# Kernel tuning notes

Hardware: AMD Instinct MI355X
Metric: run time of the kernel (lower is better)

The kernel has to match this reference:

```python
import jax, jax.numpy as jnp
import numpy as np

K = 5  # spline kernel size per dim (dim=3 -> 125 kernels)
N1, E1 = 10000, 60000
N2, E2 = 2500, 15000
N3, E3 = 625, 3750
N4, E4 = 160, 960
NC = 4  # num part classes (ShapeNet 'Pistol')


def spline_conv(x, ei, u, W, R, b):
    """SplineConv with degree-1 open B-splines, dim=3, kernel_size=K.
    x: [N, in], ei: [2, E] (src, dst), u: [E, 3] pseudo coords in [0,1],
    W: [K^3, in, out], R: [in, out] root weight, b: [out] bias.
    Mean-normalized neighborhood aggregation (norm=True) + root + bias."""
    src, dst = ei[0], ei[1]
    N, E = x.shape[0], ei.shape[1]
    v = u * (K - 1)
    k0f = jnp.clip(jnp.floor(v), 0.0, K - 2)
    f = v - k0f  # fractional offsets in [0, 1]
    k0 = k0f.astype(jnp.int32)
    # Pre-transform node features by every kernel: z[n, k, o]
    z = jnp.einsum('ni,kio->nko', x, W)
    msg = jnp.zeros((E, W.shape[2]), x.dtype)
    for b0 in (0, 1):
        for b1 in (0, 1):
            for b2 in (0, 1):
                idx = (k0[:, 0] + b0) * K * K + (k0[:, 1] + b1) * K + (k0[:, 2] + b2)
                wgt = ((f[:, 0] if b0 else 1.0 - f[:, 0]) *
                       (f[:, 1] if b1 else 1.0 - f[:, 1]) *
                       (f[:, 2] if b2 else 1.0 - f[:, 2]))
                msg = msg + wgt[:, None] * z[src, idx]
    agg = jax.ops.segment_sum(msg, dst, num_segments=N)
    deg = jax.ops.segment_sum(jnp.ones((E,), x.dtype), dst, num_segments=N)
    return agg / jnp.maximum(deg, 1.0)[:, None] + x @ R + b


def _net(x, u1, u2, u3, u4, w1, r1, b1, w12, r12, b12, w2, r2, b2, w22, r22, b22,
         w3, r3, b3, w32, r32, b32, w4, r4, b4, w42, r42, b42, w5, r5, b5,
         w6, r6, b6, w7, r7, b7, fc1w, fc1b, fc2w, fc2b,
         sk1w, sk1b, sk2w, sk2b, sk3w, sk3b, ei1, ei2, ei3, ei4, c1, c2, c3):
    elu = jax.nn.elu
    h1 = elu(spline_conv(x, ei1, u1, w1, r1, b1))
    h1 = elu(spline_conv(h1, ei1, u1, w12, r12, b12))
    h2 = jnp.concatenate([jax.ops.segment_max(h1, c1, num_segments=N2),
                          jnp.ones((N2, 1), x.dtype)], axis=1)
    h2 = elu(spline_conv(h2, ei2, u2, w2, r2, b2))
    h2 = elu(spline_conv(h2, ei2, u2, w22, r22, b22))
    h3 = jnp.concatenate([jax.ops.segment_max(h2, c2, num_segments=N3),
                          jnp.ones((N3, 1), x.dtype)], axis=1)
    h3 = elu(spline_conv(h3, ei3, u3, w3, r3, b3))
    h3 = elu(spline_conv(h3, ei3, u3, w32, r32, b32))
    h4 = jnp.concatenate([jax.ops.segment_max(h3, c3, num_segments=N4),
                          jnp.ones((N4, 1), x.dtype)], axis=1)
    h4 = elu(spline_conv(h4, ei4, u4, w4, r4, b4))
    h4 = elu(spline_conv(h4, ei4, u4, w42, r42, b42))
    h4 = elu(spline_conv(h4, ei4, u4, w42, r42, b42))  # conv42 applied twice, as in source
    h4 = elu(h4 @ fc1w + fc1b)  # dropout omitted (eval mode)
    g3 = elu(spline_conv(h4[c3] + h3 @ sk3w + sk3b, ei3, u3, w5, r5, b5))
    g2 = elu(spline_conv(g3[c2] + h2 @ sk2w + sk2b, ei2, u2, w6, r6, b6))
    g1 = elu(spline_conv(g2[c1] + h1 @ sk1w + sk1b, ei1, u1, w7, r7, b7))
    return jax.nn.log_softmax(g1 @ fc2w + fc2b, axis=1)


def setup_inputs() -> dict:
    key = jax.random.key(0)
    ks = iter(jax.random.split(key, 96))

    def nrm(shape, s=0.1):
        return jax.random.normal(next(ks), shape, jnp.float32) * s

    def edges(E, N):
        return jax.random.randint(next(ks), (2, E), 0, N, dtype=jnp.int32)

    def clus(Nl, Nn):
        # surjective cluster assignment so every pooled voxel is non-empty
        extra = jax.random.randint(next(ks), (Nl - Nn,), 0, Nn, dtype=jnp.int32)
        return jnp.concatenate([jnp.arange(Nn, dtype=jnp.int32), extra])

    d = {}
    d['x'] = nrm((N1, 1), 1.0)
    d['ei1'], d['u1'] = edges(E1, N1), jax.random.uniform(next(ks), (E1, 3), jnp.float32)
    d['ei2'], d['u2'] = edges(E2, N2), jax.random.uniform(next(ks), (E2, 3), jnp.float32)
    d['ei3'], d['u3'] = edges(E3, N3), jax.random.uniform(next(ks), (E3, 3), jnp.float32)
    d['ei4'], d['u4'] = edges(E4, N4), jax.random.uniform(next(ks), (E4, 3), jnp.float32)
    d['c1'], d['c2'], d['c3'] = clus(N1, N2), clus(N2, N3), clus(N3, N4)
    KK = K ** 3
    for name, cin, cout in [('1', 1, 64), ('12', 64, 64), ('2', 65, 64), ('22', 64, 64),
                            ('3', 65, 64), ('32', 64, 64), ('4', 65, 64), ('42', 64, 64),
                            ('5', 32, 32), ('6', 32, 32), ('7', 32, 32)]:
        d['w' + name] = nrm((KK, cin, cout))
        d['r' + name] = nrm((cin, cout))
        d['b' + name] = jnp.zeros((cout,), jnp.float32)
    d['fc1w'], d['fc1b'] = nrm((64, 32)), jnp.zeros((32,), jnp.float32)
    d['fc2w'], d['fc2b'] = nrm((32, NC)), jnp.zeros((NC,), jnp.float32)
    for s in ('1', '2', '3'):
        d['sk' + s + 'w'] = nrm((64, 32))
        d['sk' + s + 'b'] = jnp.zeros((32,), jnp.float32)
    return d


def reference(x, u1, u2, u3, u4, w1, r1, b1, w12, r12, b12, w2, r2, b2, w22, r22, b22,
              w3, r3, b3, w32, r32, b32, w4, r4, b4, w42, r42, b42, w5, r5, b5,
              w6, r6, b6, w7, r7, b7, fc1w, fc1b, fc2w, fc2b,
              sk1w, sk1b, sk2w, sk2b, sk3w, sk3b, ei1, ei2, ei3, ei4, c1, c2, c3):
    return _net(x, u1, u2, u3, u4, w1, r1, b1, w12, r12, b12, w2, r2, b2, w22, r22, b22,
                w3, r3, b3, w32, r32, b32, w4, r4, b4, w42, r42, b42, w5, r5, b5,
                w6, r6, b6, w7, r7, b7, fc1w, fc1b, fc2w, fc2b,
                sk1w, sk1b, sk2w, sk2b, sk3w, sk3b, ei1, ei2, ei3, ei4, c1, c2, c3)
```

## Files before the change

### kernel.cpp

```cpp
#include <hip/hip_runtime.h>
#include <math.h>


static const int N1 = 10000, E1 = 60000;
static const int N2 = 2500,  E2 = 15000;
static const int N3 = 625,   E3 = 3750;
static const int N4 = 160,   E4 = 960;
static const int NC = 4;
static const int CHUNK = 64;

typedef __attribute__((ext_vector_type(8))) short bfrag;
typedef __attribute__((ext_vector_type(4))) float f32x4;

__device__ __forceinline__ float eluf(float x) { return x > 0.f ? x : expm1f(x); }

__device__ __forceinline__ unsigned short bfc(float f) {
    unsigned u = __float_as_uint(f);
    return (unsigned short)((u + 0x7FFF + ((u >> 16) & 1)) >> 16);
}

struct InitArgs {
    const float* wsrc[10]; unsigned short* wdst[10];
    int cinmat[10], xs_[10], cout[10];
    long welems[10];
    long wtot;
    float* pools[3]; int pM[3];
    float* agg; int aggN4;
    int* preblk; int preN;
    int bB, bC, bD;
};

__global__ __launch_bounds__(256) void init_misc(InitArgs A) {
    const int blk = blockIdx.x, tid = threadIdx.x;
    if (blk < A.bB) {
        const long t = (long)blk * 256 + tid;
        if (t >= A.wtot) return;
        int k = 0;
        while (t >= A.welems[k]) ++k;
        const long base = k ? A.welems[k - 1] : 0;
        const long i2 = t - base;
        const int co = A.cout[k], cm = A.cinmat[k], xs = A.xs_[k];
        const int o = (int)(i2 % co);
        const long rest = i2 / co;
        const int i = (int)(rest % cm);
        const int kk = (int)(rest / cm);
        const float v = A.wsrc[k][((size_t)kk * xs + i) * co + o];
        const int KG = cm >> 3;
        A.wdst[k][(((size_t)(kk * KG + (i >> 3))) * co + o) * 8 + (i & 7)] = bfc(v);
    } else if (blk < A.bC) {
        const int t = (blk - A.bB) * 256 + tid;
        if (t >= A.pM[2]) return;
        const int p = (t < A.pM[0]) ? 0 : (t < A.pM[1] ? 1 : 2);
        const int base = p ? A.pM[p - 1] : 0;
        const int i2 = t - base;
        A.pools[p][i2] = (i2 % 65 == 64) ? 1.0f : -INFINITY;
    } else if (blk < A.bD) {
        const int t = (blk - A.bC) * 256 + tid;
        if (t < A.aggN4) ((float4*)A.agg)[t] = make_float4(0.f, 0.f, 0.f, 0.f);
    } else {
        const int t = (blk - A.bD) * 256 + tid;
        if (t < A.preN) A.preblk[t] = 0;
    }
}

struct Levels {
    const float* u[4]; const int* ei[4]; int E[4];
    int nb0[5];
    int cb0[5];
    int mc[4];
    int* ek0[4]; int* hist[4]; int* cursor[4]; float* deg[4];
    int* bchunk0[4]; int* ck0[4]; int* ccnt[4]; int* perm[4];
};

__global__ __launch_bounds__(256) void prep_all(Levels L) {
    int l = 0;
    while (l < 3 && (int)blockIdx.x >= L.nb0[l + 1]) ++l;
    const int bl = blockIdx.x - L.nb0[l];
    __shared__ int lh[64];
    const int t = threadIdx.x;
    if (t < 64) lh[t] = 0;
    __syncthreads();
    const int e = bl * 256 + t;
    if (e < L.E[l]) {
        int b = 0;
        #pragma unroll
        for (int d = 0; d < 3; ++d) {
            const float v = L.u[l][e * 3 + d] * 4.0f;
            const float kf = fminf(fmaxf(floorf(v), 0.f), 3.f);
            b = (b << 2) | (int)kf;
        }
        L.ek0[l][e] = b;
        atomicAdd(&lh[b], 1);
        atomicAdd(&L.deg[l][L.ei[l][L.E[l] + e]], 1.0f);
    }
    __syncthreads();
    if (t < 64 && lh[t]) atomicAdd(&L.hist[l][t], lh[t]);
}

__global__ void scan_all(Levels L) {
    const int l = blockIdx.x;
    __shared__ int sb[65];
    const int t = threadIdx.x;
    if (t == 0) {
        int cc = 0;
        for (int b = 0; b < 64; ++b) { sb[b] = cc; cc += (L.hist[l][b] + CHUNK - 1) / CHUNK; }
        sb[64] = cc;
    }
    __syncthreads();
    L.bchunk0[l][t] = sb[t];
    if (t == 0) L.bchunk0[l][64] = sb[64];
}

__global__ void fill_chunks_all(Levels L) {
    int l = 0;
    while (l < 3 && (int)blockIdx.x >= L.cb0[l + 1]) ++l;
    const int c = (blockIdx.x - L.cb0[l]) * 256 + threadIdx.x;
    if (c >= L.mc[l]) return;
    const int* bchunk0 = L.bchunk0[l];
    if (c >= bchunk0[64]) { L.ccnt[l][c] = 0; L.ck0[l][c] = 0; return; }
    int lo = 0, hi = 64;
    while (hi - lo > 1) { int m = (lo + hi) >> 1; if (bchunk0[m] <= c) lo = m; else hi = m; }
    const int j = c - bchunk0[lo];
    L.ck0[l][c] = lo;
    L.ccnt[l][c] = min(CHUNK, L.hist[l][lo] - j * CHUNK);
}

__global__ __launch_bounds__(256) void scatter_all(Levels L) {
    int l = 0;
    while (l < 3 && (int)blockIdx.x >= L.nb0[l + 1]) ++l;
    const int bl = blockIdx.x - L.nb0[l];
    __shared__ int lh[64], lbase[64];
    const int t = threadIdx.x;
    if (t < 64) lh[t] = 0;
    __syncthreads();
    const int e = bl * 256 + t;
    int b = -1, r = 0;
    if (e < L.E[l]) { b = L.ek0[l][e]; r = atomicAdd(&lh[b], 1); }
    __syncthreads();
    if (t < 64) lbase[t] = lh[t] ? atomicAdd(&L.cursor[l][t], lh[t]) : 0;
    __syncthreads();
    if (e < L.E[l]) L.perm[l][L.bchunk0[l][b] * CHUNK + lbase[b] + r] = e;
}

template<int CINMAT, int COUT, bool HAS_ONES>
__global__ __launch_bounds__(256) void bucket_gemm(
        const float* __restrict__ x, const int* __restrict__ ei, const float* __restrict__ u,
        const unsigned short* __restrict__ Wt, const float* __restrict__ Wf,
        const int* __restrict__ perm, const int* __restrict__ ck0, const int* __restrict__ ccnt,
        float* __restrict__ agg, int E) {
    constexpr int ALDA = CINMAT + 8;
    constexpr int KG   = CINMAT / 8;
    constexpr int NT   = COUT / 16;
    constexpr int HALVES = CINMAT / 32;
    constexpr int XS   = CINMAT + (HAS_ONES ? 1 : 0);
    constexpr int IT   = CINMAT / 4;

    __shared__ unsigned short A0s[64 * ALDA], A1s[64 * ALDA];
    __shared__ float gS[64 * 4], sS[64 * 2];
    __shared__ int srcS[64], dstS[64];
    __shared__ float WonesS[HAS_ONES ? 8 * COUT : 4];

    const int chunk = blockIdx.x;
    const int cnt = ccnt[chunk];
    if (cnt == 0) return;
    const int b = ck0[chunk];
    const int kbase = ((b >> 4) & 3) * 25 + ((b >> 2) & 3) * 5 + (b & 3);
    const int cstart = chunk * CHUNK;
    const int tid = threadIdx.x;

    if (tid < CHUNK) {
        const int e = tid;
        const int pe = (e < cnt) ? perm[cstart + e] : -1;
        int sv = -1, dv = 0;
        float g0 = 0, g1 = 0, g2 = 0, g3 = 0, s0 = 0, s1 = 0;
        if (pe >= 0) {
            sv = ei[pe]; dv = ei[E + pe];
            float f[3];
            #pragma unroll
            for (int d2 = 0; d2 < 3; ++d2) {
                const float v = u[pe * 3 + d2] * 4.f;
                const float kf = fminf(fmaxf(floorf(v), 0.f), 3.f);
                f[d2] = v - kf;
            }
            g0 = (1.f - f[0]) * (1.f - f[1]); g1 = (1.f - f[0]) * f[1];
            g2 = f[0] * (1.f - f[1]);         g3 = f[0] * f[1];
            s0 = 1.f - f[2]; s1 = f[2];
        }
        srcS[e] = sv; dstS[e] = dv;
        gS[e * 4 + 0] = g0; gS[e * 4 + 1] = g1; gS[e * 4 + 2] = g2; gS[e * 4 + 3] = g3;
        sS[e * 2 + 0] = s0; sS[e * 2 + 1] = s1;
    }
    if (HAS_ONES) {
        for (int t2 = tid; t2 < 8 * COUT; t2 += 256) {
            const int c = t2 / COUT, o = t2 % COUT;
            const int koff = ((c >> 2) & 1) * 25 + ((c >> 1) & 1) * 5 + (c & 1);
            WonesS[t2] = Wf[((size_t)(kbase + koff) * XS + CINMAT) * COUT + o];
        }
    }
    __syncthreads();

    {
        const int e  = tid >> 2;
        const int ib = (tid & 3) * IT;
        const int sv = srcS[e];
        const float sc0 = sS[e * 2], sc1 = sS[e * 2 + 1];
        #pragma unroll
        for (int j = 0; j < IT; j += 2) {
            float x0 = 0.f, x1 = 0.f;
            if (sv >= 0) {
                x0 = x[(size_t)sv * XS + ib + j];
                x1 = x[(size_t)sv * XS + ib + j + 1];
            }
            const unsigned p0 = bfc(x0 * sc0) | ((unsigned)bfc(x1 * sc0) << 16);
            const unsigned p1 = bfc(x0 * sc1) | ((unsigned)bfc(x1 * sc1) << 16);
            *(unsigned*)&A0s[e * ALDA + ib + j] = p0;
            *(unsigned*)&A1s[e * ALDA + ib + j] = p1;
        }
    }
    __syncthreads();

    const int lane = tid & 63;
    const int wid  = tid >> 6;
    const int m0   = wid * 16;
    const int arow = m0 + (lane & 15);
    const int kg   = lane >> 4;
    const int ocol = lane & 15;

    f32x4 acc[4][NT];
    #pragma unroll
    for (int q = 0; q < 4; ++q)
        #pragma unroll
        for (int nt = 0; nt < NT; ++nt) acc[q][nt] = (f32x4){0.f, 0.f, 0.f, 0.f};

    #pragma unroll
    for (int q = 0; q < 4; ++q) {
        #pragma unroll
        for (int b2 = 0; b2 < 2; ++b2) {
            const unsigned short* Ab = b2 ? A1s : A0s;
            const int koff = (q >> 1) * 25 + (q & 1) * 5 + b2;
            #pragma unroll
            for (int hf = 0; hf < HALVES; ++hf) {
                const bfrag a = *(const bfrag*)(Ab + arow * ALDA + hf * 32 + kg * 8);
                const int krow = (kbase + koff) * KG + hf * 4 + kg;
                #pragma unroll
                for (int nt = 0; nt < NT; ++nt) {
                    const bfrag bb = *(const bfrag*)(Wt + ((size_t)krow * COUT + nt * 16 + ocol) * 8);
                    acc[q][nt] = __builtin_amdgcn_mfma_f32_16x16x32_bf16(a, bb, acc[q][nt], 0, 0, 0);
                }
            }
        }
    }

    const int grp = lane >> 4;
    #pragma unroll
    for (int nt = 0; nt < NT; ++nt) {
        const int o = nt * 16 + ocol;
        float wo[8];
        if (HAS_ONES) {
            #pragma unroll
            for (int c = 0; c < 8; ++c) wo[c] = WonesS[c * COUT + o];
        }
        #pragma unroll
        for (int r = 0; r < 4; ++r) {
            const int e = m0 + grp * 4 + r;
            if (e < cnt) {
                const float g0 = gS[e * 4 + 0], g1 = gS[e * 4 + 1];
                const float g2 = gS[e * 4 + 2], g3 = gS[e * 4 + 3];
                float v = g0 * acc[0][nt][r] + g1 * acc[1][nt][r] +
                          g2 * acc[2][nt][r] + g3 * acc[3][nt][r];
                if (HAS_ONES) {
                    const float s0v = sS[e * 2], s1v = sS[e * 2 + 1];
                    v += g0 * (s0v * wo[0] + s1v * wo[1]) + g1 * (s0v * wo[2] + s1v * wo[3]) +
                         g2 * (s0v * wo[4] + s1v * wo[5]) + g3 * (s0v * wo[6] + s1v * wo[7]);
                }
                atomicAdd(&agg[(size_t)dstS[e] * COUT + o], v);
            }
        }
    }
}

template<int CIN, int COUT, int BLK>
__global__ __launch_bounds__(BLK) void bucket_edge(
        const float* __restrict__ x, const int* __restrict__ ei, const float* __restrict__ u,
        const float* __restrict__ W, const int* __restrict__ perm,
        const int* __restrict__ ck0, const int* __restrict__ ccnt,
        float* __restrict__ agg, int E) {
    constexpr int CINP = (CIN + 3) & ~3;
    __shared__ float xs[CHUNK * CINP];
    __shared__ float wgt[CHUNK * 8];
    __shared__ int pel[CHUNK], srcl[CHUNK], dstl[CHUNK];

    const int chunk = blockIdx.x;
    const int cnt = ccnt[chunk];
    if (cnt == 0) return;
    const int b = ck0[chunk];
    const int kbase = ((b >> 4) & 3) * 25 + ((b >> 2) & 3) * 5 + (b & 3);
    const int cstart = chunk * CHUNK;
    const int tid = threadIdx.x;

    for (int e = tid; e < CHUNK; e += BLK) {
        if (e < cnt) {
            const int pe = perm[cstart + e];
            pel[e] = pe; srcl[e] = ei[pe]; dstl[e] = ei[E + pe];
        } else { pel[e] = -1; srcl[e] = -1; dstl[e] = -1; }
    }
    __syncthreads();
    for (int t2 = tid; t2 < CHUNK * 8; t2 += BLK) {
        const int e = t2 >> 3, c = t2 & 7;
        float w = 0.f;
        const int pe = pel[e];
        if (pe >= 0) {
            w = 1.f;
            #pragma unroll
            for (int d = 0; d < 3; ++d) {
                const float v = u[pe * 3 + d] * 4.0f;
                const float kf = fminf(fmaxf(floorf(v), 0.f), 3.f);
                const float fr = v - kf;
                const int bd = (c >> (2 - d)) & 1;
                w *= bd ? fr : 1.f - fr;
            }
        }
        wgt[t2] = w;
    }
    for (int t2 = tid; t2 < CHUNK * CINP; t2 += BLK) {
        const int e = t2 / CINP, i = t2 - e * CINP;
        const int s = srcl[e];
        xs[t2] = (s >= 0 && i < CIN) ? x[(size_t)s * CIN + i] : 0.f;
    }
    __syncthreads();

    const int lane = tid & 63;
    const int wid  = tid >> 6;
    const int o = lane;
    const int ehbase = wid * 8;

    float acc2[8][8];
    #pragma unroll
    for (int c = 0; c < 8; ++c)
        #pragma unroll
        for (int e = 0; e < 8; ++e) acc2[c][e] = 0.f;

    for (int i = 0; i < CIN; ++i) {
        float xr1[8];
        #pragma unroll
        for (int e = 0; e < 8; ++e) xr1[e] = xs[(ehbase + e) * CINP + i];
        #pragma unroll
        for (int c = 0; c < 8; ++c) {
            const int off = ((c >> 2) & 1) * 25 + ((c >> 1) & 1) * 5 + (c & 1);
            const float w0 = W[(size_t)(kbase + off) * (CIN * COUT) + (size_t)i * COUT + o];
            #pragma unroll
            for (int e = 0; e < 8; ++e) acc2[c][e] += xr1[e] * w0;
        }
    }
    #pragma unroll
    for (int e = 0; e < 8; ++e) {
        const int ge = ehbase + e;
        if (ge < cnt) {
            float a = 0.f;
            #pragma unroll
            for (int c = 0; c < 8; ++c) a += wgt[ge * 8 + c] * acc2[c][e];
            atomicAdd(&agg[(size_t)dstl[ge] * COUT + o], a);
        }
    }
}

enum { NODE_PLAIN = 0, NODE_SEGMAX = 1, NODE_LSM = 2 };

template<int CIN, int COUT, int MODE>
__global__ void spline_node_f(const float* __restrict__ x, float* __restrict__ agg,
                              const float* __restrict__ deg, const float* __restrict__ R,
                              const float* __restrict__ b, float* __restrict__ out, int N,
                              const int* __restrict__ cl, float* __restrict__ pool,
                              const float* __restrict__ fcw, const float* __restrict__ fcb,
                              float* __restrict__ lout) {
    constexpr int NPB = 256 / COUT;
    const int lane = threadIdx.x % COUT;
    const int grp  = threadIdx.x / COUT;
    const int n = blockIdx.x * NPB + grp;
    if (n >= N) return;
    const float d = fmaxf(deg[n], 1.f);
    const size_t idx = (size_t)n * COUT + lane;
    float s = agg[idx] / d + b[lane];
    agg[idx] = 0.f;
    const float* xs = x + (size_t)n * CIN;
    #pragma unroll 4
    for (int i = 0; i < CIN; ++i) s += xs[i] * R[i * COUT + lane];
    const float val = eluf(s);
    if (MODE != NODE_LSM) out[idx] = val;
    if (MODE == NODE_SEGMAX) {
        float* addr = pool + (size_t)cl[n] * 65 + lane;
        if (val >= 0.f) atomicMax((int*)addr, __float_as_int(val));
        else            atomicMin((unsigned int*)addr, __float_as_uint(val));
    }
    if (MODE == NODE_LSM) {
        float p[NC];
        #pragma unroll
        for (int o = 0; o < NC; ++o) p[o] = val * fcw[lane * NC + o];
        #pragma unroll
        for (int m = 16; m >= 1; m >>= 1)
            #pragma unroll
            for (int o = 0; o < NC; ++o) p[o] += __shfl_xor(p[o], m, 32);
        #pragma unroll
        for (int o = 0; o < NC; ++o) p[o] += fcb[o];
        const float mx = fmaxf(fmaxf(p[0], p[1]), fmaxf(p[2], p[3]));
        float se = 0.f;
        #pragma unroll
        for (int o = 0; o < NC; ++o) se += expf(p[o] - mx);
        const float lg = logf(se);
        if (lane < NC) lout[(size_t)n * NC + lane] = p[lane] - mx - lg;
    }
}

__global__ void skip_gather(const float* __restrict__ up, const int* __restrict__ cl,
                            const float* __restrict__ h, const float* __restrict__ skw,
                            const float* __restrict__ skb, float* __restrict__ out, int N) {
    const int lane = threadIdx.x & 31;
    const int grp  = threadIdx.x >> 5;
    const int n = blockIdx.x * 8 + grp;
    if (n >= N) return;
    float s = up[(size_t)cl[n] * 32 + lane] + skb[lane];
    const float* hs = h + (size_t)n * 64;
    #pragma unroll 4
    for (int i = 0; i < 64; ++i) s += hs[i] * skw[i * 32 + lane];
    out[(size_t)n * 32 + lane] = s;
}

__global__ void linear_elu_64_32(const float* __restrict__ x, const float* __restrict__ w,
                                 const float* __restrict__ b, float* __restrict__ out, int N) {
    const int lane = threadIdx.x & 31;
    const int grp  = threadIdx.x >> 5;
    const int n = blockIdx.x * 8 + grp;
    if (n >= N) return;
    float s = b[lane];
    const float* xs = x + (size_t)n * 64;
    #pragma unroll 4
    for (int i = 0; i < 64; ++i) s += xs[i] * w[i * 32 + lane];
    out[(size_t)n * 32 + lane] = eluf(s);
}

struct HLevel {
    const int* ei; const float* u; int E; int maxchunks;
    int *ek0, *hist, *cursor, *bchunk0, *ck0, *ccnt, *perm;
    float* deg;
};

extern "C" void kernel_launch(void* const* d_in, const int* in_sizes, int n_in,
                              void* d_out, int out_size, void* d_ws, size_t ws_size,
                              hipStream_t stream) {
    const float* x    = (const float*)d_in[0];
    const int*   ei1  = (const int*)  d_in[1];
    const float* u1   = (const float*)d_in[2];
    const int*   ei2  = (const int*)  d_in[3];
    const float* u2   = (const float*)d_in[4];
    const int*   ei3  = (const int*)  d_in[5];
    const float* u3   = (const float*)d_in[6];
    const int*   ei4  = (const int*)  d_in[7];
    const float* u4   = (const float*)d_in[8];
    const int*   c1   = (const int*)  d_in[9];
    const int*   c2   = (const int*)  d_in[10];
    const int*   c3   = (const int*)  d_in[11];
    const float *w1  = (const float*)d_in[12], *r1  = (const float*)d_in[13], *b1  = (const float*)d_in[14];
    const float *w12 = (const float*)d_in[15], *r12 = (const float*)d_in[16], *b12 = (const float*)d_in[17];
    const float *w2  = (const float*)d_in[18], *r2  = (const float*)d_in[19], *b2  = (const float*)d_in[20];
    const float *w22 = (const float*)d_in[21], *r22 = (const float*)d_in[22], *b22 = (const float*)d_in[23];
    const float *w3  = (const float*)d_in[24], *r3  = (const float*)d_in[25], *b3  = (const float*)d_in[26];
    const float *w32 = (const float*)d_in[27], *r32 = (const float*)d_in[28], *b32 = (const float*)d_in[29];
    const float *w4  = (const float*)d_in[30], *r4  = (const float*)d_in[31], *b4  = (const float*)d_in[32];
    const float *w42 = (const float*)d_in[33], *r42 = (const float*)d_in[34], *b42 = (const float*)d_in[35];
    const float *w5  = (const float*)d_in[36], *r5  = (const float*)d_in[37], *b5  = (const float*)d_in[38];
    const float *w6  = (const float*)d_in[39], *r6  = (const float*)d_in[40], *b6  = (const float*)d_in[41];
    const float *w7  = (const float*)d_in[42], *r7  = (const float*)d_in[43], *b7  = (const float*)d_in[44];
    const float *fc1w = (const float*)d_in[45], *fc1b = (const float*)d_in[46];
    const float *fc2w = (const float*)d_in[47], *fc2b = (const float*)d_in[48];
    const float *sk1w = (const float*)d_in[49], *sk1b = (const float*)d_in[50];
    const float *sk2w = (const float*)d_in[51], *sk2b = (const float*)d_in[52];
    const float *sk3w = (const float*)d_in[53], *sk3b = (const float*)d_in[54];
    float* out = (float*)d_out;

    char* wsb = (char*)d_ws;
    size_t off = 0;
    auto alloc = [&](size_t bytes) {
        void* p = wsb + off; off = (off + bytes + 255) & ~(size_t)255; return p;
    };
    auto allocF = [&](size_t n) { return (float*)alloc(n * 4); };
    auto allocI = [&](size_t n) { return (int*)alloc(n * 4); };
    auto allocH = [&](size_t n) { return (unsigned short*)alloc(n * 2); };

    float* h1a  = allocF((size_t)N1 * 64);
    float* h1   = allocF((size_t)N1 * 64);
    float* h2in = allocF((size_t)N2 * 65);
    float* h2a  = allocF((size_t)N2 * 64);
    float* h2   = allocF((size_t)N2 * 64);
    float* h3in = allocF((size_t)N3 * 65);
    float* h3a  = allocF((size_t)N3 * 64);
    float* h3   = allocF((size_t)N3 * 64);
    float* h4in = allocF((size_t)N4 * 65);
    float* h4a  = allocF((size_t)N4 * 64);
    float* h4b  = allocF((size_t)N4 * 64);
    float* h4c  = allocF((size_t)N4 * 64);
    float* h4   = allocF((size_t)N4 * 32);
    float* g3in = allocF((size_t)N3 * 32);
    float* g3   = allocF((size_t)N3 * 32);
    float* g2in = allocF((size_t)N2 * 32);
    float* g2   = allocF((size_t)N2 * 32);
    float* g1in = allocF((size_t)N1 * 32);
    float* agg  = allocF((size_t)N1 * 64);

    const size_t SZ64 = (size_t)125 * 8 * 64 * 8;
    const size_t SZ32 = (size_t)125 * 4 * 32 * 8;
    unsigned short* t12 = allocH(SZ64);
    unsigned short* t22 = allocH(SZ64);
    unsigned short* t32 = allocH(SZ64);
    unsigned short* t42 = allocH(SZ64);
    unsigned short* t2  = allocH(SZ64);
    unsigned short* t3  = allocH(SZ64);
    unsigned short* t4  = allocH(SZ64);
    unsigned short* t5  = allocH(SZ32);
    unsigned short* t6  = allocH(SZ32);
    unsigned short* t7  = allocH(SZ32);

    HLevel L[4];
    const int*   eis[4] = {ei1, ei2, ei3, ei4};
    const float* us [4] = {u1, u2, u3, u4};
    const int    Es [4] = {E1, E2, E3, E4};
    const int    Ns [4] = {N1, N2, N3, N4};

    int preN = 0;
    for (int l = 0; l < 4; ++l) preN += 128 + Ns[l];
    int* preblk = allocI(preN);
    {
        int c = 0;
        for (int l = 0; l < 4; ++l) {
            L[l].ei = eis[l]; L[l].u = us[l]; L[l].E = Es[l];
            L[l].maxchunks = (Es[l] + CHUNK - 1) / CHUNK + 64;
            L[l].hist = preblk + c; L[l].cursor = preblk + c + 64;
            L[l].deg = (float*)(preblk + c + 128);
            c += 128 + Ns[l];
            L[l].ek0     = allocI(Es[l]);
            L[l].bchunk0 = allocI(65);
            L[l].ck0     = allocI(L[l].maxchunks);
            L[l].ccnt    = allocI(L[l].maxchunks);
            L[l].perm    = allocI((size_t)L[l].maxchunks * CHUNK);
        }
    }

    InitArgs IA;
    {
        const float* srcs[10] = {w12, w22, w32, w42, w2, w3, w4, w5, w6, w7};
        unsigned short* dsts[10] = {t12, t22, t32, t42, t2, t3, t4, t5, t6, t7};
        const int cms[10] = {64,64,64,64,64,64,64,32,32,32};
        const int xss[10] = {64,64,64,64,65,65,65,32,32,32};
        const int cos[10] = {64,64,64,64,64,64,64,32,32,32};
        long cum = 0;
        for (int k = 0; k < 10; ++k) {
            IA.wsrc[k] = srcs[k]; IA.wdst[k] = dsts[k];
            IA.cinmat[k] = cms[k]; IA.xs_[k] = xss[k]; IA.cout[k] = cos[k];
            cum += (long)125 * cms[k] * cos[k];
            IA.welems[k] = cum;
        }
        IA.wtot = cum;
        IA.pools[0] = h2in; IA.pools[1] = h3in; IA.pools[2] = h4in;
        IA.pM[0] = N2 * 65; IA.pM[1] = N2 * 65 + N3 * 65; IA.pM[2] = N2 * 65 + N3 * 65 + N4 * 65;
        IA.agg = agg; IA.aggN4 = N1 * 64 / 4;
        IA.preblk = preblk; IA.preN = preN;
        const int bA = (int)((IA.wtot + 255) / 256);
        const int bB = (IA.pM[2] + 255) / 256;
        const int bC = (IA.aggN4 + 255) / 256;
        const int bD = (preN + 255) / 256;
        IA.bB = bA; IA.bC = bA + bB; IA.bD = bA + bB + bC;
        init_misc<<<bA + bB + bC + bD, 256, 0, stream>>>(IA);
    }

    Levels DL;
    {
        int nb = 0, cb = 0;
        for (int l = 0; l < 4; ++l) {
            DL.u[l] = L[l].u; DL.ei[l] = L[l].ei; DL.E[l] = L[l].E;
            DL.nb0[l] = nb; nb += (L[l].E + 255) / 256;
            DL.cb0[l] = cb; cb += (L[l].maxchunks + 255) / 256;
            DL.mc[l] = L[l].maxchunks;
            DL.ek0[l] = L[l].ek0; DL.hist[l] = L[l].hist; DL.cursor[l] = L[l].cursor;
            DL.deg[l] = L[l].deg; DL.bchunk0[l] = L[l].bchunk0;
            DL.ck0[l] = L[l].ck0; DL.ccnt[l] = L[l].ccnt; DL.perm[l] = L[l].perm;
        }
        DL.nb0[4] = nb; DL.cb0[4] = cb;
        prep_all<<<nb, 256, 0, stream>>>(DL);
        scan_all<<<4, 64, 0, stream>>>(DL);
        fill_chunks_all<<<cb, 256, 0, stream>>>(DL);
        scatter_all<<<nb, 256, 0, stream>>>(DL);
    }

    bucket_edge<1, 64, 512><<<L[0].maxchunks, 512, 0, stream>>>(
        x, L[0].ei, L[0].u, w1, L[0].perm, L[0].ck0, L[0].ccnt, agg, L[0].E);
    spline_node_f<1, 64, NODE_PLAIN><<<(N1 + 3) / 4, 256, 0, stream>>>(
        x, agg, L[0].deg, r1, b1, h1a, N1, nullptr, nullptr, nullptr, nullptr, nullptr);

    bucket_gemm<64, 64, false><<<L[0].maxchunks, 256, 0, stream>>>(
        h1a, L[0].ei, L[0].u, t12, nullptr, L[0].perm, L[0].ck0, L[0].ccnt, agg, L[0].E);
    spline_node_f<64, 64, NODE_SEGMAX><<<(N1 + 3) / 4, 256, 0, stream>>>(
        h1a, agg, L[0].deg, r12, b12, h1, N1, c1, h2in, nullptr, nullptr, nullptr);

    bucket_gemm<64, 64, true><<<L[1].maxchunks, 256, 0, stream>>>(
        h2in, L[1].ei, L[1].u, t2, w2, L[1].perm, L[1].ck0, L[1].ccnt, agg, L[1].E);
    spline_node_f<65, 64, NODE_PLAIN><<<(N2 + 3) / 4, 256, 0, stream>>>(
        h2in, agg, L[1].deg, r2, b2, h2a, N2, nullptr, nullptr, nullptr, nullptr, nullptr);
    bucket_gemm<64, 64, false><<<L[1].maxchunks, 256, 0, stream>>>(
        h2a, L[1].ei, L[1].u, t22, nullptr, L[1].perm, L[1].ck0, L[1].ccnt, agg, L[1].E);
    spline_node_f<64, 64, NODE_SEGMAX><<<(N2 + 3) / 4, 256, 0, stream>>>(
        h2a, agg, L[1].deg, r22, b22, h2, N2, c2, h3in, nullptr, nullptr, nullptr);

    bucket_gemm<64, 64, true><<<L[2].maxchunks, 256, 0, stream>>>(
        h3in, L[2].ei, L[2].u, t3, w3, L[2].perm, L[2].ck0, L[2].ccnt, agg, L[2].E);
    spline_node_f<65, 64, NODE_PLAIN><<<(N3 + 3) / 4, 256, 0, stream>>>(
        h3in, agg, L[2].deg, r3, b3, h3a, N3, nullptr, nullptr, nullptr, nullptr, nullptr);
    bucket_gemm<64, 64, false><<<L[2].maxchunks, 256, 0, stream>>>(
        h3a, L[2].ei, L[2].u, t32, nullptr, L[2].perm, L[2].ck0, L[2].ccnt, agg, L[2].E);
    spline_node_f<64, 64, NODE_SEGMAX><<<(N3 + 3) / 4, 256, 0, stream>>>(
        h3a, agg, L[2].deg, r32, b32, h3, N3, c3, h4in, nullptr, nullptr, nullptr);

    bucket_gemm<64, 64, true><<<L[3].maxchunks, 256, 0, stream>>>(
        h4in, L[3].ei, L[3].u, t4, w4, L[3].perm, L[3].ck0, L[3].ccnt, agg, L[3].E);
    spline_node_f<65, 64, NODE_PLAIN><<<(N4 + 3) / 4, 256, 0, stream>>>(
        h4in, agg, L[3].deg, r4, b4, h4a, N4, nullptr, nullptr, nullptr, nullptr, nullptr);
    bucket_gemm<64, 64, false><<<L[3].maxchunks, 256, 0, stream>>>(
        h4a, L[3].ei, L[3].u, t42, nullptr, L[3].perm, L[3].ck0, L[3].ccnt, agg, L[3].E);
    spline_node_f<64, 64, NODE_PLAIN><<<(N4 + 3) / 4, 256, 0, stream>>>(
        h4a, agg, L[3].deg, r42, b42, h4b, N4, nullptr, nullptr, nullptr, nullptr, nullptr);
    bucket_gemm<64, 64, false><<<L[3].maxchunks, 256, 0, stream>>>(
        h4b, L[3].ei, L[3].u, t42, nullptr, L[3].perm, L[3].ck0, L[3].ccnt, agg, L[3].E);
    spline_node_f<64, 64, NODE_PLAIN><<<(N4 + 3) / 4, 256, 0, stream>>>(
        h4b, agg, L[3].deg, r42, b42, h4c, N4, nullptr, nullptr, nullptr, nullptr, nullptr);

    linear_elu_64_32<<<(N4 + 7) / 8, 256, 0, stream>>>(h4c, fc1w, fc1b, h4, N4);

    skip_gather<<<(N3 + 7) / 8, 256, 0, stream>>>(h4, c3, h3, sk3w, sk3b, g3in, N3);
    bucket_gemm<32, 32, false><<<L[2].maxchunks, 256, 0, stream>>>(
        g3in, L[2].ei, L[2].u, t5, nullptr, L[2].perm, L[2].ck0, L[2].ccnt, agg, L[2].E);
    spline_node_f<32, 32, NODE_PLAIN><<<(N3 + 7) / 8, 256, 0, stream>>>(
        g3in, agg, L[2].deg, r5, b5, g3, N3, nullptr, nullptr, nullptr, nullptr, nullptr);

    skip_gather<<<(N2 + 7) / 8, 256, 0, stream>>>(g3, c2, h2, sk2w, sk2b, g2in, N2);
    bucket_gemm<32, 32, false><<<L[1].maxchunks, 256, 0, stream>>>(
        g2in, L[1].ei, L[1].u, t6, nullptr, L[1].perm, L[1].ck0, L[1].ccnt, agg, L[1].E);
    spline_node_f<32, 32, NODE_PLAIN><<<(N2 + 7) / 8, 256, 0, stream>>>(
        g2in, agg, L[1].deg, r6, b6, g2, N2, nullptr, nullptr, nullptr, nullptr, nullptr);

    skip_gather<<<(N1 + 7) / 8, 256, 0, stream>>>(g2, c1, h1, sk1w, sk1b, g1in, N1);
    bucket_gemm<32, 32, false><<<L[0].maxchunks, 256, 0, stream>>>(
        g1in, L[0].ei, L[0].u, t7, nullptr, L[0].perm, L[0].ck0, L[0].ccnt, agg, L[0].E);
    spline_node_f<32, 32, NODE_LSM><<<(N1 + 7) / 8, 256, 0, stream>>>(
        g1in, agg, L[0].deg, r7, b7, nullptr, N1, nullptr, nullptr, fc2w, fc2b, out);
}
```

Before: 294.6 us.

## Fuse conv1 into prep, merge fill/scatter/node1, fold fc1 into node kernel

The first spline conv (scalar input) is now computed directly per edge and output channel inside the preprocessing kernel, which removes the bucket_edge kernel. Chunk filling, perm scatter and the layer-1 node update are merged into one multi-role launch, and the fc1 linear+ELU is folded into the last spline node kernel through a shared-memory row buffer. This cuts several kernel launches and their global-memory round trips. The cost is more atomics on agg for conv1 and heterogeneous blocks within single launches. The fused fc1 reads rowbuf with no barrier, so it relies on each 64-lane group being a single wavefront.

```diff
diff --git a/kernel.cpp b/kernel.cpp
--- a/kernel.cpp
+++ b/kernel.cpp
@@ -72,29 +72,54 @@
     int* bchunk0[4]; int* ck0[4]; int* ccnt[4]; int* perm[4];
 };
 
-__global__ __launch_bounds__(256) void prep_all(Levels L) {
-    int l = 0;
-    while (l < 3 && (int)blockIdx.x >= L.nb0[l + 1]) ++l;
-    const int bl = blockIdx.x - L.nb0[l];
+__global__ __launch_bounds__(256) void prep_conv1(Levels L, const float* __restrict__ x,
+                                                  const float* __restrict__ w1,
+                                                  float* __restrict__ agg, int nbTot) {
     __shared__ int lh[64];
-    const int t = threadIdx.x;
-    if (t < 64) lh[t] = 0;
-    __syncthreads();
-    const int e = bl * 256 + t;
-    if (e < L.E[l]) {
-        int b = 0;
+    const int tid = threadIdx.x;
+    if ((int)blockIdx.x < nbTot) {
+        int l = 0;
+        while (l < 3 && (int)blockIdx.x >= L.nb0[l + 1]) ++l;
+        const int bl = blockIdx.x - L.nb0[l];
+        if (tid < 64) lh[tid] = 0;
+        __syncthreads();
+        const int e = bl * 256 + tid;
+        if (e < L.E[l]) {
+            int b = 0;
+            #pragma unroll
+            for (int d = 0; d < 3; ++d) {
+                const float v = L.u[l][e * 3 + d] * 4.0f;
+                const float kf = fminf(fmaxf(floorf(v), 0.f), 3.f);
+                b = (b << 2) | (int)kf;
+            }
+            L.ek0[l][e] = b;
+            atomicAdd(&lh[b], 1);
+            atomicAdd(&L.deg[l][L.ei[l][L.E[l] + e]], 1.0f);
+        }
+        __syncthreads();
+        if (tid < 64 && lh[tid]) atomicAdd(&L.hist[l][tid], lh[tid]);
+    } else {
+        const int t = (blockIdx.x - nbTot) * 256 + tid;
+        const int e = t >> 6, o = t & 63;
+        if (e >= E1) return;
+        const int src = L.ei[0][e], dst = L.ei[0][E1 + e];
+        float f[3]; int kb = 0;
         #pragma unroll
         for (int d = 0; d < 3; ++d) {
-            const float v = L.u[l][e * 3 + d] * 4.0f;
+            const float v = L.u[0][e * 3 + d] * 4.0f;
             const float kf = fminf(fmaxf(floorf(v), 0.f), 3.f);
-            b = (b << 2) | (int)kf;
-        }
-        L.ek0[l][e] = b;
-        atomicAdd(&lh[b], 1);
-        atomicAdd(&L.deg[l][L.ei[l][L.E[l] + e]], 1.0f);
-    }
-    __syncthreads();
-    if (t < 64 && lh[t]) atomicAdd(&L.hist[l][t], lh[t]);
+            f[d] = v - kf; kb = kb * 5 + (int)kf;
+        }
+        float s = 0.f;
+        #pragma unroll
+        for (int c = 0; c < 8; ++c) {
+            const int b0 = (c >> 2) & 1, b1 = (c >> 1) & 1, b2 = c & 1;
+            const float wgt = (b0 ? f[0] : 1.f - f[0]) * (b1 ? f[1] : 1.f - f[1]) *
+                              (b2 ? f[2] : 1.f - f[2]);
+            s += wgt * w1[(size_t)(kb + b0 * 25 + b1 * 5 + b2) * 64 + o];
+        }
+        atomicAdd(&agg[(size_t)dst * 64 + o], x[src] * s);
+    }
 }
 
 __global__ void scan_all(Levels L) {
@@ -111,35 +136,52 @@
     if (t == 0) L.bchunk0[l][64] = sb[64];
 }
 
-__global__ void fill_chunks_all(Levels L) {
-    int l = 0;
-    while (l < 3 && (int)blockIdx.x >= L.cb0[l + 1]) ++l;
-    const int c = (blockIdx.x - L.cb0[l]) * 256 + threadIdx.x;
-    if (c >= L.mc[l]) return;
-    const int* bchunk0 = L.bchunk0[l];
-    if (c >= bchunk0[64]) { L.ccnt[l][c] = 0; L.ck0[l][c] = 0; return; }
-    int lo = 0, hi = 64;
-    while (hi - lo > 1) { int m = (lo + hi) >> 1; if (bchunk0[m] <= c) lo = m; else hi = m; }
-    const int j = c - bchunk0[lo];
-    L.ck0[l][c] = lo;
-    L.ccnt[l][c] = min(CHUNK, L.hist[l][lo] - j * CHUNK);
-}
-
-__global__ __launch_bounds__(256) void scatter_all(Levels L) {
-    int l = 0;
-    while (l < 3 && (int)blockIdx.x >= L.nb0[l + 1]) ++l;
-    const int bl = blockIdx.x - L.nb0[l];
+__global__ __launch_bounds__(256) void fill_scatter_node1(
+        Levels L, const float* __restrict__ x, float* __restrict__ agg,
+        const float* __restrict__ r1, const float* __restrict__ b1,
+        float* __restrict__ h1a, int cbTot, int nbTot) {
     __shared__ int lh[64], lbase[64];
-    const int t = threadIdx.x;
-    if (t < 64) lh[t] = 0;
-    __syncthreads();
-    const int e = bl * 256 + t;
-    int b = -1, r = 0;
-    if (e < L.E[l]) { b = L.ek0[l][e]; r = atomicAdd(&lh[b], 1); }
-    __syncthreads();
-    if (t < 64) lbase[t] = lh[t] ? atomicAdd(&L.cursor[l][t], lh[t]) : 0;
-    __syncthreads();
-    if (e < L.E[l]) L.perm[l][L.bchunk0[l][b] * CHUNK + lbase[b] + r] = e;
+    const int tid = threadIdx.x;
+    const int blk = blockIdx.x;
+    if (blk < cbTot) {
+        int l = 0;
+        while (l < 3 && blk >= L.cb0[l + 1]) ++l;
+        const int c = (blk - L.cb0[l]) * 256 + tid;
+        if (c >= L.mc[l]) return;
+        const int* bchunk0 = L.bchunk0[l];
+        if (c >= bchunk0[64]) { L.ccnt[l][c] = 0; L.ck0[l][c] = 0; return; }
+        int lo = 0, hi = 64;
+        while (hi - lo > 1) { int m = (lo + hi) >> 1; if (bchunk0[m] <= c) lo = m; else hi = m; }
+        const int j = c - bchunk0[lo];
+        L.ck0[l][c] = lo;
+        L.ccnt[l][c] = min(CHUNK, L.hist[l][lo] - j * CHUNK);
+    } else if (blk < cbTot + nbTot) {
+        const int fb = blk - cbTot;
+        int l = 0;
+        while (l < 3 && fb >= L.nb0[l + 1]) ++l;
+        const int bl = fb - L.nb0[l];
+        if (tid < 64) lh[tid] = 0;
+        __syncthreads();
+        const int e = bl * 256 + tid;
+        int b = -1, r = 0;
+        if (e < L.E[l]) { b = L.ek0[l][e]; r = atomicAdd(&lh[b], 1); }
+        __syncthreads();
+        if (tid < 64) lbase[tid] = lh[tid] ? atomicAdd(&L.cursor[l][tid], lh[tid]) : 0;
+        __syncthreads();
+        if (e < L.E[l]) L.perm[l][L.bchunk0[l][b] * CHUNK + lbase[b] + r] = e;
+    } else {
+        const int nb = blk - cbTot - nbTot;
+        const int lane = tid & 63;
+        const int grp  = tid >> 6;
+        const int n = nb * 4 + grp;
+        if (n >= N1) return;
+        const float d = fmaxf(L.deg[0][n], 1.f);
+        const size_t idx = (size_t)n * 64 + lane;
+        float s = agg[idx] / d + b1[lane];
+        agg[idx] = 0.f;
+        s += x[n] * r1[lane];
+        h1a[idx] = eluf(s);
+    }
 }
 
 template<int CINMAT, int COUT, bool HAS_ONES>
@@ -279,101 +321,17 @@
     }
 }
 
-template<int CIN, int COUT, int BLK>
-__global__ __launch_bounds__(BLK) void bucket_edge(
-        const float* __restrict__ x, const int* __restrict__ ei, const float* __restrict__ u,
-        const float* __restrict__ W, const int* __restrict__ perm,
-        const int* __restrict__ ck0, const int* __restrict__ ccnt,
-        float* __restrict__ agg, int E) {
-    constexpr int CINP = (CIN + 3) & ~3;
-    __shared__ float xs[CHUNK * CINP];
-    __shared__ float wgt[CHUNK * 8];
-    __shared__ int pel[CHUNK], srcl[CHUNK], dstl[CHUNK];
-
-    const int chunk = blockIdx.x;
-    const int cnt = ccnt[chunk];
-    if (cnt == 0) return;
-    const int b = ck0[chunk];
-    const int kbase = ((b >> 4) & 3) * 25 + ((b >> 2) & 3) * 5 + (b & 3);
-    const int cstart = chunk * CHUNK;
-    const int tid = threadIdx.x;
-
-    for (int e = tid; e < CHUNK; e += BLK) {
-        if (e < cnt) {
-            const int pe = perm[cstart + e];
-            pel[e] = pe; srcl[e] = ei[pe]; dstl[e] = ei[E + pe];
-        } else { pel[e] = -1; srcl[e] = -1; dstl[e] = -1; }
-    }
-    __syncthreads();
-    for (int t2 = tid; t2 < CHUNK * 8; t2 += BLK) {
-        const int e = t2 >> 3, c = t2 & 7;
-        float w = 0.f;
-        const int pe = pel[e];
-        if (pe >= 0) {
-            w = 1.f;
-            #pragma unroll
-            for (int d = 0; d < 3; ++d) {
-                const float v = u[pe * 3 + d] * 4.0f;
-                const float kf = fminf(fmaxf(floorf(v), 0.f), 3.f);
-                const float fr = v - kf;
-                const int bd = (c >> (2 - d)) & 1;
-                w *= bd ? fr : 1.f - fr;
-            }
-        }
-        wgt[t2] = w;
-    }
-    for (int t2 = tid; t2 < CHUNK * CINP; t2 += BLK) {
-        const int e = t2 / CINP, i = t2 - e * CINP;
-        const int s = srcl[e];
-        xs[t2] = (s >= 0 && i < CIN) ? x[(size_t)s * CIN + i] : 0.f;
-    }
-    __syncthreads();
-
-    const int lane = tid & 63;
-    const int wid  = tid >> 6;
-    const int o = lane;
-    const int ehbase = wid * 8;
-
-    float acc2[8][8];
-    #pragma unroll
-    for (int c = 0; c < 8; ++c)
-        #pragma unroll
-        for (int e = 0; e < 8; ++e) acc2[c][e] = 0.f;
-
-    for (int i = 0; i < CIN; ++i) {
-        float xr1[8];
-        #pragma unroll
-        for (int e = 0; e < 8; ++e) xr1[e] = xs[(ehbase + e) * CINP + i];
-        #pragma unroll
-        for (int c = 0; c < 8; ++c) {
-            const int off = ((c >> 2) & 1) * 25 + ((c >> 1) & 1) * 5 + (c & 1);
-            const float w0 = W[(size_t)(kbase + off) * (CIN * COUT) + (size_t)i * COUT + o];
-            #pragma unroll
-            for (int e = 0; e < 8; ++e) acc2[c][e] += xr1[e] * w0;
-        }
-    }
-    #pragma unroll
-    for (int e = 0; e < 8; ++e) {
-        const int ge = ehbase + e;
-        if (ge < cnt) {
-            float a = 0.f;
-            #pragma unroll
-            for (int c = 0; c < 8; ++c) a += wgt[ge * 8 + c] * acc2[c][e];
-            atomicAdd(&agg[(size_t)dstl[ge] * COUT + o], a);
-        }
-    }
-}
-
-enum { NODE_PLAIN = 0, NODE_SEGMAX = 1, NODE_LSM = 2 };
+enum { NODE_PLAIN = 0, NODE_SEGMAX = 1, NODE_FC1 = 2, NODE_LSM = 3 };
 
 template<int CIN, int COUT, int MODE>
 __global__ void spline_node_f(const float* __restrict__ x, float* __restrict__ agg,
                               const float* __restrict__ deg, const float* __restrict__ R,
                               const float* __restrict__ b, float* __restrict__ out, int N,
                               const int* __restrict__ cl, float* __restrict__ pool,
-                              const float* __restrict__ fcw, const float* __restrict__ fcb,
-                              float* __restrict__ lout) {
+                              const float* __restrict__ fw, const float* __restrict__ fb2,
+                              float* __restrict__ fout) {
     constexpr int NPB = 256 / COUT;
+    __shared__ float rowbuf[NPB][COUT];
     const int lane = threadIdx.x % COUT;
     const int grp  = threadIdx.x / COUT;
     const int n = blockIdx.x * NPB + grp;
@@ -386,28 +344,37 @@
     #pragma unroll 4
     for (int i = 0; i < CIN; ++i) s += xs[i] * R[i * COUT + lane];
     const float val = eluf(s);
-    if (MODE != NODE_LSM) out[idx] = val;
+    if (MODE == NODE_PLAIN || MODE == NODE_SEGMAX) out[idx] = val;
     if (MODE == NODE_SEGMAX) {
         float* addr = pool + (size_t)cl[n] * 65 + lane;
         if (val >= 0.f) atomicMax((int*)addr, __float_as_int(val));
         else            atomicMin((unsigned int*)addr, __float_as_uint(val));
     }
+    if (MODE == NODE_FC1) {
+        rowbuf[grp][lane] = val;
+        if (lane < 32) {
+            float s2 = fb2[lane];
+            #pragma unroll 4
+            for (int i = 0; i < 64; ++i) s2 += rowbuf[grp][i] * fw[i * 32 + lane];
+            fout[(size_t)n * 32 + lane] = eluf(s2);
+        }
+    }
     if (MODE == NODE_LSM) {
         float p[NC];
         #pragma unroll
-        for (int o = 0; o < NC; ++o) p[o] = val * fcw[lane * NC + o];
+        for (int o = 0; o < NC; ++o) p[o] = val * fw[lane * NC + o];
         #pragma unroll
         for (int m = 16; m >= 1; m >>= 1)
             #pragma unroll
             for (int o = 0; o < NC; ++o) p[o] += __shfl_xor(p[o], m, 32);
         #pragma unroll
-        for (int o = 0; o < NC; ++o) p[o] += fcb[o];
+        for (int o = 0; o < NC; ++o) p[o] += fb2[o];
         const float mx = fmaxf(fmaxf(p[0], p[1]), fmaxf(p[2], p[3]));
         float se = 0.f;
         #pragma unroll
         for (int o = 0; o < NC; ++o) se += expf(p[o] - mx);
         const float lg = logf(se);
-        if (lane < NC) lout[(size_t)n * NC + lane] = p[lane] - mx - lg;
+        if (lane < NC) fout[(size_t)n * NC + lane] = p[lane] - mx - lg;
     }
 }
 
@@ -423,19 +390,6 @@
     #pragma unroll 4
     for (int i = 0; i < 64; ++i) s += hs[i] * skw[i * 32 + lane];
     out[(size_t)n * 32 + lane] = s;
-}
-
-__global__ void linear_elu_64_32(const float* __restrict__ x, const float* __restrict__ w,
-                                 const float* __restrict__ b, float* __restrict__ out, int N) {
-    const int lane = threadIdx.x & 31;
-    const int grp  = threadIdx.x >> 5;
-    const int n = blockIdx.x * 8 + grp;
-    if (n >= N) return;
-    float s = b[lane];
-    const float* xs = x + (size_t)n * 64;
-    #pragma unroll 4
-    for (int i = 0; i < 64; ++i) s += xs[i] * w[i * 32 + lane];
-    out[(size_t)n * 32 + lane] = eluf(s);
 }
 
 struct HLevel {
@@ -497,7 +451,6 @@
     float* h4in = allocF((size_t)N4 * 65);
     float* h4a  = allocF((size_t)N4 * 64);
     float* h4b  = allocF((size_t)N4 * 64);
-    float* h4c  = allocF((size_t)N4 * 64);
     float* h4   = allocF((size_t)N4 * 32);
     float* g3in = allocF((size_t)N3 * 32);
     float* g3   = allocF((size_t)N3 * 32);
@@ -572,28 +525,25 @@
     }
 
     Levels DL;
+    int nbTot = 0, cbTot = 0;
     {
-        int nb = 0, cb = 0;
         for (int l = 0; l < 4; ++l) {
             DL.u[l] = L[l].u; DL.ei[l] = L[l].ei; DL.E[l] = L[l].E;
-            DL.nb0[l] = nb; nb += (L[l].E + 255) / 256;
-            DL.cb0[l] = cb; cb += (L[l].maxchunks + 255) / 256;
+            DL.nb0[l] = nbTot; nbTot += (L[l].E + 255) / 256;
+            DL.cb0[l] = cbTot; cbTot += (L[l].maxchunks + 255) / 256;
             DL.mc[l] = L[l].maxchunks;
             DL.ek0[l] = L[l].ek0; DL.hist[l] = L[l].hist; DL.cursor[l] = L[l].cursor;
             DL.deg[l] = L[l].deg; DL.bchunk0[l] = L[l].bchunk0;
             DL.ck0[l] = L[l].ck0; DL.ccnt[l] = L[l].ccnt; DL.perm[l] = L[l].perm;
         }
-        DL.nb0[4] = nb; DL.cb0[4] = cb;
-        prep_all<<<nb, 256, 0, stream>>>(DL);
+        DL.nb0[4] = nbTot; DL.cb0[4] = cbTot;
+        const int conv1B = (E1 * 64) / 256;
+        prep_conv1<<<nbTot + conv1B, 256, 0, stream>>>(DL, x, w1, agg, nbTot);
         scan_all<<<4, 64, 0, stream>>>(DL);
-        fill_chunks_all<<<cb, 256, 0, stream>>>(DL);
-        scatter_all<<<nb, 256, 0, stream>>>(DL);
-    }
-
-    bucket_edge<1, 64, 512><<<L[0].maxchunks, 512, 0, stream>>>(
-        x, L[0].ei, L[0].u, w1, L[0].perm, L[0].ck0, L[0].ccnt, agg, L[0].E);
-    spline_node_f<1, 64, NODE_PLAIN><<<(N1 + 3) / 4, 256, 0, stream>>>(
-        x, agg, L[0].deg, r1, b1, h1a, N1, nullptr, nullptr, nullptr, nullptr, nullptr);
+        const int n1B = (N1 + 3) / 4;
+        fill_scatter_node1<<<cbTot + nbTot + n1B, 256, 0, stream>>>(
+            DL, x, agg, r1, b1, h1a, cbTot, nbTot);
+    }
 
     bucket_gemm<64, 64, false><<<L[0].maxchunks, 256, 0, stream>>>(
         h1a, L[0].ei, L[0].u, t12, nullptr, L[0].perm, L[0].ck0, L[0].ccnt, agg, L[0].E);
@@ -628,10 +578,8 @@
         h4a, agg, L[3].deg, r42, b42, h4b, N4, nullptr, nullptr, nullptr, nullptr, nullptr);
     bucket_gemm<64, 64, false><<<L[3].maxchunks, 256, 0, stream>>>(
         h4b, L[3].ei, L[3].u, t42, nullptr, L[3].perm, L[3].ck0, L[3].ccnt, agg, L[3].E);
-    spline_node_f<64, 64, NODE_PLAIN><<<(N4 + 3) / 4, 256, 0, stream>>>(
-        h4b, agg, L[3].deg, r42, b42, h4c, N4, nullptr, nullptr, nullptr, nullptr, nullptr);
-
-    linear_elu_64_32<<<(N4 + 7) / 8, 256, 0, stream>>>(h4c, fc1w, fc1b, h4, N4);
+    spline_node_f<64, 64, NODE_FC1><<<(N4 + 3) / 4, 256, 0, stream>>>(
+        h4b, agg, L[3].deg, r42, b42, nullptr, N4, nullptr, nullptr, fc1w, fc1b, h4);
 
     skip_gather<<<(N3 + 7) / 8, 256, 0, stream>>>(h4, c3, h3, sk3w, sk3b, g3in, N3);
     bucket_gemm<32, 32, false><<<L[2].maxchunks, 256, 0, stream>>>(
```

Result: faster. 284.1 us (-3.5%).
